# Kernel tuning notes

Measured on AMD Instinct MI355X. Metric: run time of the kernel, lower is better.

## Reference

```python
import jax, jax.numpy as jnp
import numpy as np

HEAD_SIZE = 64
EMB_SIZE = 1024
B, N = 4, 4096


def setup_inputs() -> dict:
    key = jax.random.key(0)
    kx, kk, kq, kv = jax.random.split(key, 4)
    x = jax.random.normal(kx, (B, N, EMB_SIZE), dtype=jnp.float32)
    # nn.Linear(emb, head, bias=False): weight [head, emb]; y = x @ W.T
    s = 1.0 / np.sqrt(EMB_SIZE)
    Wk = jax.random.uniform(kk, (HEAD_SIZE, EMB_SIZE), jnp.float32, -s, s)
    Wq = jax.random.uniform(kq, (HEAD_SIZE, EMB_SIZE), jnp.float32, -s, s)
    Wv = jax.random.uniform(kv, (HEAD_SIZE, EMB_SIZE), jnp.float32, -s, s)
    return {"x": x, "Wk": Wk, "Wq": Wq, "Wv": Wv}


def reference(x, Wk, Wq, Wv):
    # k, q, v: [B, N, H]
    k = jnp.einsum("bne,he->bnh", x, Wk)
    q = jnp.einsum("bne,he->bnh", x, Wq)
    v = jnp.einsum("bne,he->bnh", x, Wv)
    scale = HEAD_SIZE ** -0.5
    aff = jnp.einsum("bqh,bkh->bqk", q, k) * scale  # [B, N, N]
    aff = jax.nn.softmax(aff, axis=2)
    # dropout rate is 0.0 -> identity
    return jnp.einsum("bqk,bkh->bqh", aff, v)
```

## Files before the change

kernel.cpp:

```cpp
#include <hip/hip_runtime.h>

#define NB   4
#define SEQ  4096
#define EMB  1024
#define HS   64

typedef __attribute__((ext_vector_type(8))) short bf16x8;
typedef __attribute__((ext_vector_type(4))) float f32x4;

__device__ inline unsigned short f2bf(float f) {
  unsigned int u = __float_as_uint(f);
  u += 0x7fffu + ((u >> 16) & 1u);
  return (unsigned short)(u >> 16);
}
__device__ inline float bf2f(unsigned short h) {
  return __uint_as_float(((unsigned int)h) << 16);
}
__device__ inline int swzi64(int row, int c) {
  return row * 64 + ((c ^ (row & 7)) << 3);
}
__device__ inline int swzi32(int row, int c) {
  return row * 32 + ((c ^ ((row >> 1) & 3)) << 3);
}
__device__ inline int swzi128(int row, int c) {
  return row * 128 + ((c ^ (row & 7)) << 3);
}
__device__ inline void gld16(const unsigned short* g, unsigned short* l) {
  __builtin_amdgcn_global_load_lds(
      (const __attribute__((address_space(1))) void*)g,
      (__attribute__((address_space(3))) void*)l, 16, 0, 0);
}

__global__ __launch_bounds__(256) void wprep(
    const float* __restrict__ Wk, const float* __restrict__ Wq,
    const float* __restrict__ Wv,
    unsigned short* __restrict__ Wh, unsigned short* __restrict__ Wl) {
  int i = blockIdx.x * 256 + threadIdx.x;
  int e = i >> 8, c = i & 255;
  float4 v;
  float sc = 1.0f;
  if (e < 64)       { v = ((const float4*)Wq)[e * 256 + c];
                      sc = 0.18033688011112042f; }
  else if (e < 128)   v = ((const float4*)Wk)[(e - 64) * 256 + c];
  else                v = ((const float4*)Wv)[(e - 128) * 256 + c];
  v.x *= sc; v.y *= sc; v.z *= sc; v.w *= sc;
  ushort4 hv, lv;
  hv.x = f2bf(v.x); lv.x = f2bf(v.x - bf2f(hv.x));
  hv.y = f2bf(v.y); lv.y = f2bf(v.y - bf2f(hv.y));
  hv.z = f2bf(v.z); lv.z = f2bf(v.z - bf2f(hv.z));
  hv.w = f2bf(v.w); lv.w = f2bf(v.w - bf2f(hv.w));
  *(ushort4*)&Wh[i * 4] = hv;
  *(ushort4*)&Wl[i * 4] = lv;
}

#define XhSp(p) ((unsigned short*)(SM + (p) * 2048))
#define XlSp(p) ((unsigned short*)(SM + 4096 + (p) * 2048))
#define WhSp(p) ((unsigned short*)(SM + 8192 + (p) * 12288))
#define WlSp(p) ((unsigned short*)(SM + 32768 + (p) * 12288))

__global__ __launch_bounds__(256) void qkv_x1(
    const float* __restrict__ x,
    const unsigned short* __restrict__ Wh, const unsigned short* __restrict__ Wl,
    unsigned short* __restrict__ qh, unsigned short* __restrict__ ql,
    unsigned short* __restrict__ kh, unsigned short* __restrict__ kl,
    unsigned short* __restrict__ vt) {
  __shared__ __align__(16) unsigned char SM[57344];

  const int t  = threadIdx.x;
  const int l  = t & 63;
  const int li = l & 15;
  const int g  = l >> 4;
  const int w  = t >> 6;
  const int m0 = blockIdx.x * 32;
  const int b  = m0 >> 12;
  const int n0 = m0 & 4095;

  const int xrow = t >> 3;
  const float* xp = x + (m0 + xrow) * EMB + (t & 7) * 4;
  const int xaddr = xrow * 32 + ((((t & 7) >> 1) ^ ((xrow >> 1) & 3)) << 3)
                    + (t & 1) * 4;

  const int wconst = (l >> 2) * EMB + (((l & 3) ^ ((l >> 3) & 3)) << 3);

  f32x4 acc[2][3];
#pragma unroll
  for (int i = 0; i < 2; ++i)
#pragma unroll
    for (int j = 0; j < 3; ++j) acc[i][j] = (f32x4){0.f, 0.f, 0.f, 0.f};

  const int rA0 = li, rA1 = 16 + li;
  const int rB0 = 48 * w + li, rB1 = rB0 + 16, rB2 = rB0 + 32;

  auto issueW = [&](int s, int p) {
    const int ko = s * 32;
#pragma unroll
    for (int i = 0; i < 3; ++i) {
      const int seg = 3 * w + i;
      gld16(Wh + 16 * seg * EMB + wconst + ko, WhSp(p) + seg * 512);
      gld16(Wl + 16 * seg * EMB + wconst + ko, WlSp(p) + seg * 512);
    }
  };
  auto writeX = [&](float4 v, int p) {
    unsigned short h0 = f2bf(v.x), h1 = f2bf(v.y), h2 = f2bf(v.z), h3 = f2bf(v.w);
    unsigned short e0 = f2bf(v.x - bf2f(h0)), e1 = f2bf(v.y - bf2f(h1));
    unsigned short e2 = f2bf(v.z - bf2f(h2)), e3 = f2bf(v.w - bf2f(h3));
    int2 hv, lv;
    hv.x = (int)((unsigned)h0 | ((unsigned)h1 << 16));
    hv.y = (int)((unsigned)h2 | ((unsigned)h3 << 16));
    lv.x = (int)((unsigned)e0 | ((unsigned)e1 << 16));
    lv.y = (int)((unsigned)e2 | ((unsigned)e3 << 16));
    *(int2*)&XhSp(p)[xaddr] = hv;
    *(int2*)&XlSp(p)[xaddr] = lv;
  };

  float4 px = *(const float4*)xp;
  issueW(0, 0);
  writeX(px, 0);
  px = *(const float4*)(xp + 32);
  __syncthreads();

  for (int s = 0; s < 32; ++s) {
    const int p = s & 1;
    if (s < 31) {
      issueW(s + 1, p ^ 1);
      writeX(px, p ^ 1);
      if (s < 30) px = *(const float4*)(xp + (s + 2) * 32);
    } else {
      asm volatile("s_waitcnt vmcnt(0)" ::: "memory");
    }
    __builtin_amdgcn_sched_barrier(0);

    bf16x8 ah0 = *(const bf16x8*)&XhSp(p)[swzi32(rA0, g)];
    bf16x8 ah1 = *(const bf16x8*)&XhSp(p)[swzi32(rA1, g)];
    bf16x8 al0 = *(const bf16x8*)&XlSp(p)[swzi32(rA0, g)];
    bf16x8 al1 = *(const bf16x8*)&XlSp(p)[swzi32(rA1, g)];
    bf16x8 bh0 = *(const bf16x8*)&WhSp(p)[swzi32(rB0, g)];
    bf16x8 bh1 = *(const bf16x8*)&WhSp(p)[swzi32(rB1, g)];
    bf16x8 bh2 = *(const bf16x8*)&WhSp(p)[swzi32(rB2, g)];
    bf16x8 bl0 = *(const bf16x8*)&WlSp(p)[swzi32(rB0, g)];
    bf16x8 bl1 = *(const bf16x8*)&WlSp(p)[swzi32(rB1, g)];
    bf16x8 bl2 = *(const bf16x8*)&WlSp(p)[swzi32(rB2, g)];

    __builtin_amdgcn_s_setprio(1);
    acc[0][0] = __builtin_amdgcn_mfma_f32_16x16x32_bf16(ah0, bh0, acc[0][0], 0,0,0);
    acc[0][0] = __builtin_amdgcn_mfma_f32_16x16x32_bf16(ah0, bl0, acc[0][0], 0,0,0);
    acc[0][0] = __builtin_amdgcn_mfma_f32_16x16x32_bf16(al0, bh0, acc[0][0], 0,0,0);
    acc[0][1] = __builtin_amdgcn_mfma_f32_16x16x32_bf16(ah0, bh1, acc[0][1], 0,0,0);
    acc[0][1] = __builtin_amdgcn_mfma_f32_16x16x32_bf16(ah0, bl1, acc[0][1], 0,0,0);
    acc[0][1] = __builtin_amdgcn_mfma_f32_16x16x32_bf16(al0, bh1, acc[0][1], 0,0,0);
    acc[0][2] = __builtin_amdgcn_mfma_f32_16x16x32_bf16(ah0, bh2, acc[0][2], 0,0,0);
    acc[0][2] = __builtin_amdgcn_mfma_f32_16x16x32_bf16(ah0, bl2, acc[0][2], 0,0,0);
    acc[0][2] = __builtin_amdgcn_mfma_f32_16x16x32_bf16(al0, bh2, acc[0][2], 0,0,0);
    acc[1][0] = __builtin_amdgcn_mfma_f32_16x16x32_bf16(ah1, bh0, acc[1][0], 0,0,0);
    acc[1][0] = __builtin_amdgcn_mfma_f32_16x16x32_bf16(ah1, bl0, acc[1][0], 0,0,0);
    acc[1][0] = __builtin_amdgcn_mfma_f32_16x16x32_bf16(al1, bh0, acc[1][0], 0,0,0);
    acc[1][1] = __builtin_amdgcn_mfma_f32_16x16x32_bf16(ah1, bh1, acc[1][1], 0,0,0);
    acc[1][1] = __builtin_amdgcn_mfma_f32_16x16x32_bf16(ah1, bl1, acc[1][1], 0,0,0);
    acc[1][1] = __builtin_amdgcn_mfma_f32_16x16x32_bf16(al1, bh1, acc[1][1], 0,0,0);
    acc[1][2] = __builtin_amdgcn_mfma_f32_16x16x32_bf16(ah1, bh2, acc[1][2], 0,0,0);
    acc[1][2] = __builtin_amdgcn_mfma_f32_16x16x32_bf16(ah1, bl2, acc[1][2], 0,0,0);
    acc[1][2] = __builtin_amdgcn_mfma_f32_16x16x32_bf16(al1, bh2, acc[1][2], 0,0,0);
    __builtin_amdgcn_s_setprio(0);

    asm volatile("s_waitcnt lgkmcnt(0)" ::: "memory");
    __builtin_amdgcn_s_barrier();
    __builtin_amdgcn_sched_barrier(0);
  }

#pragma unroll
  for (int i = 0; i < 2; ++i)
#pragma unroll
    for (int j = 0; j < 3; ++j) {
      const int H3 = 48 * w + 16 * j + li;
#pragma unroll
      for (int r = 0; r < 4; ++r) {
        const int mrow = 16 * i + 4 * g + r;
        const float vv = acc[i][j][r];
        if (H3 < 64) {
          const unsigned short hb = f2bf(vv);
          const int off = (b * SEQ + n0 + mrow) * HS + H3;
          qh[off] = hb; ql[off] = f2bf(vv - bf2f(hb));
        } else if (H3 < 128) {
          const unsigned short hb = f2bf(vv);
          const int off = (b * SEQ + n0 + mrow) * HS + (H3 - 64);
          kh[off] = hb; kl[off] = f2bf(vv - bf2f(hb));
        } else {
          vt[(b * HS + (H3 - 128)) * SEQ + n0 + mrow] = f2bf(vv);
        }
      }
    }
}

__global__ __launch_bounds__(1024) void attn_mfma(
    const unsigned short* __restrict__ qh, const unsigned short* __restrict__ ql,
    const unsigned short* __restrict__ kh, const unsigned short* __restrict__ kl,
    const unsigned short* __restrict__ vt, float* __restrict__ out) {
  __shared__ __align__(16) unsigned char SM[155648];
  unsigned short* const PtS = (unsigned short*)(SM + 114688);

  const int t  = threadIdx.x;
  const int l  = t & 63;
  const int li = l & 15;
  const int g  = l >> 4;
  const int w  = t >> 6;
  const int qg = w & 1;
  const int kf = w >> 1;
  const int ks2 = (w >> 1) & 3;
  const int hh  = w >> 3;
  const int b  = blockIdx.y;
  const int q0 = blockIdx.x << 6;

  bf16x8 qfh[2][2], qfl[2][2];
#pragma unroll
  for (int qs = 0; qs < 2; ++qs) {
    const unsigned short* qrh = qh + (b * SEQ + q0 + 32 * qg + 16 * qs + li) * HS;
    const unsigned short* qrl = ql + (b * SEQ + q0 + 32 * qg + 16 * qs + li) * HS;
    qfh[qs][0] = *(const bf16x8*)&qrh[8 * g];
    qfh[qs][1] = *(const bf16x8*)&qrh[32 + 8 * g];
    qfl[qs][0] = *(const bf16x8*)&qrl[8 * g];
    qfl[qs][1] = *(const bf16x8*)&qrl[32 + 8 * g];
  }

  const int kconst = (l >> 3) * HS + (((l & 7) ^ (l >> 3)) << 3);
  const int rowl = l >> 4, slot = l & 15;
  const int vc = (w & 1) ? rowl * SEQ + ((slot ^ (4 + rowl)) << 3)
                         : rowl * SEQ + ((slot ^ rowl) << 3);
  const unsigned short* khB = kh + b * SEQ * HS;
  const unsigned short* klB = kl + b * SEQ * HS;
  const unsigned short* vtB = vt + b * HS * SEQ;

  f32x4 O[2][2];
#pragma unroll
  for (int i = 0; i < 2; ++i) {
    O[i][0] = (f32x4){0.f, 0.f, 0.f, 0.f};
    O[i][1] = (f32x4){0.f, 0.f, 0.f, 0.f};
  }
  float lp0 = 0.f, lp1 = 0.f;

  const int slabW = qg + 2 * (kf >> 1);
  const int cW = 2 * (kf & 1) + (g >> 1);
  const int subW = (g & 1) << 2;

  auto stage = [&](int it, int pK, int vb) {
    const int kt0 = it << 7;
    unsigned short* const KhP = (unsigned short*)(SM + pK * 16384);
    unsigned short* const KlP = (unsigned short*)(SM + 32768 + pK * 16384);
    unsigned short* const VtP = (unsigned short*)(SM + 65536 + vb * 16384);
    gld16(khB + (kt0 + 8 * w) * HS + kconst, KhP + w * 512);
    gld16(klB + (kt0 + 8 * w) * HS + kconst, KlP + w * 512);
    gld16(vtB + 4 * w * SEQ + kt0 + vc, VtP + w * 512);
  };

  auto PV = [&](int par, int vb) {
    unsigned short* const PtP = PtS + (qg + 2 * ks2) * 2560 + par * 1280;
    unsigned short* const VtP = (unsigned short*)(SM + 65536 + vb * 16384);
    bf16x8 pb0 = *(const bf16x8*)&PtP[li * 40 + ((g ^ (li & 3)) << 3)];
    const int r1 = 16 + li;
    bf16x8 pb1 = *(const bf16x8*)&PtP[r1 * 40 + ((g ^ (r1 & 3)) << 3)];
    __builtin_amdgcn_s_setprio(1);
#pragma unroll
    for (int ht2 = 0; ht2 < 2; ++ht2) {
      const int vrow = 32 * hh + 16 * ht2 + li;
      bf16x8 va = *(const bf16x8*)&VtP[swzi128(vrow, 4 * ks2 + g)];
      O[ht2][0] = __builtin_amdgcn_mfma_f32_16x16x32_bf16(va, pb0, O[ht2][0], 0,0,0);
      O[ht2][1] = __builtin_amdgcn_mfma_f32_16x16x32_bf16(va, pb1, O[ht2][1], 0,0,0);
    }
    __builtin_amdgcn_s_setprio(0);
  };

  stage(0, 0, 0);
  __syncthreads();

  int vbn = 1;
  int vbp = 2;
  for (int it = 0; it < 32; ++it) {
    const int p = it & 1;
    if (it < 31) stage(it + 1, p ^ 1, vbn);

    unsigned short* const KhS = (unsigned short*)(SM + p * 16384);
    unsigned short* const KlS = (unsigned short*)(SM + 32768 + p * 16384);

    f32x4 S[2];
    S[0] = (f32x4){-32.f, -32.f, -32.f, -32.f};
    S[1] = (f32x4){-32.f, -32.f, -32.f, -32.f};
    __builtin_amdgcn_s_setprio(1);
#pragma unroll
    for (int khf = 0; khf < 2; ++khf) {
      const int row = 16 * kf + li;
      bf16x8 akh = *(const bf16x8*)&KhS[swzi64(row, 4 * khf + g)];
      bf16x8 akl = *(const bf16x8*)&KlS[swzi64(row, 4 * khf + g)];
      S[0] = __builtin_amdgcn_mfma_f32_16x16x32_bf16(akh, qfh[0][khf], S[0], 0,0,0);
      S[0] = __builtin_amdgcn_mfma_f32_16x16x32_bf16(akh, qfl[0][khf], S[0], 0,0,0);
      S[0] = __builtin_amdgcn_mfma_f32_16x16x32_bf16(akl, qfh[0][khf], S[0], 0,0,0);
      S[1] = __builtin_amdgcn_mfma_f32_16x16x32_bf16(akh, qfh[1][khf], S[1], 0,0,0);
      S[1] = __builtin_amdgcn_mfma_f32_16x16x32_bf16(akh, qfl[1][khf], S[1], 0,0,0);
      S[1] = __builtin_amdgcn_mfma_f32_16x16x32_bf16(akl, qfh[1][khf], S[1], 0,0,0);
    }
    __builtin_amdgcn_s_setprio(0);

    if (it > 0) PV(p ^ 1, vbp);

#pragma unroll
    for (int qs = 0; qs < 2; ++qs) {
      unsigned pu[4];
      float ls = 0.f;
#pragma unroll
      for (int r = 0; r < 4; ++r) {
        const float pe = exp2f(S[qs][r]);
        pu[r] = __float_as_uint(pe);
        ls += __uint_as_float(pu[r] & 0xffff0000u);
      }
      if (qs == 0) lp0 += ls; else lp1 += ls;
      const unsigned p01 = __builtin_amdgcn_perm(pu[1], pu[0], 0x07060302u);
      const unsigned p23 = __builtin_amdgcn_perm(pu[3], pu[2], 0x07060302u);
      const int qrow = 16 * qs + li;
      const int addr = qrow * 40 + (((cW ^ (qrow & 3))) << 3) + subW;
      int2 pv; pv.x = (int)p01; pv.y = (int)p23;
      *(int2*)&PtS[slabW * 2560 + p * 1280 + addr] = pv;
    }

    __syncthreads();

    vbn = (vbn == 2) ? 0 : vbn + 1;
    vbp = (vbp == 2) ? 0 : vbp + 1;
  }

  PV(1, 1);

  lp0 += __shfl_xor(lp0, 16); lp0 += __shfl_xor(lp0, 32);
  lp1 += __shfl_xor(lp1, 16); lp1 += __shfl_xor(lp1, 32);

  float* const OTm = (float*)SM;
  float* const Lm  = (float*)(SM + 65536);
#pragma unroll
  for (int ht2 = 0; ht2 < 2; ++ht2)
#pragma unroll
    for (int qs = 0; qs < 2; ++qs) {
      float4 o4;
      o4.x = O[ht2][qs][0]; o4.y = O[ht2][qs][1];
      o4.z = O[ht2][qs][2]; o4.w = O[ht2][qs][3];
      *(float4*)&OTm[(((qg * 2 + hh) * 4 + ks2) << 10)
                     + (16 * qs + li) * 32 + 16 * ht2 + 4 * g] = o4;
    }
  if (g == 0) { Lm[w * 32 + li] = lp0; Lm[w * 32 + 16 + li] = lp1; }
  __syncthreads();

  {
    const int q = t >> 4, hseg = (t & 15) << 2;
    const int qq = q & 31, qgf = q >> 5;
    const int hhf = hseg >> 5, hsub = hseg & 31;
    float lF = 0.f;
#pragma unroll
    for (int kff = 0; kff < 8; ++kff) lF += Lm[(qgf + 2 * kff) * 32 + qq];
    float4 a = {0.f, 0.f, 0.f, 0.f};
#pragma unroll
    for (int k2 = 0; k2 < 4; ++k2) {
      const float* Ob = OTm + (((qgf * 2 + hhf) * 4 + k2) << 10) + qq * 32 + hsub;
      float4 u = *(const float4*)Ob;
      a.x += u.x; a.y += u.y; a.z += u.z; a.w += u.w;
    }
    const float inv = 1.f / lF;
    a.x *= inv; a.y *= inv; a.z *= inv; a.w *= inv;
    *(float4*)(out + (b * SEQ + q0 + q) * HS + hseg) = a;
  }
}

extern "C" void kernel_launch(void* const* d_in, const int* in_sizes, int n_in,
                              void* d_out, int out_size, void* d_ws,
                              size_t ws_size, hipStream_t stream) {
  const float* x  = (const float*)d_in[0];
  const float* Wk = (const float*)d_in[1];
  const float* Wq = (const float*)d_in[2];
  const float* Wv = (const float*)d_in[3];
  float* out = (float*)d_out;

  unsigned short* us = (unsigned short*)d_ws;
  unsigned short* qh = us + 0 * (1 << 20);
  unsigned short* ql = us + 1 * (1 << 20);
  unsigned short* kh = us + 2 * (1 << 20);
  unsigned short* kl = us + 3 * (1 << 20);
  unsigned short* vt = us + 4 * (1 << 20);
  unsigned short* Wh = us + 5 * (1 << 20);
  unsigned short* Wl = Wh + 192 * 1024;

  wprep<<<192, 256, 0, stream>>>(Wk, Wq, Wv, Wh, Wl);
  qkv_x1<<<512, 256, 0, stream>>>(x, Wh, Wl, qh, ql, kh, kl, vt);
  attn_mfma<<<dim3(64, NB), 1024, 0, stream>>>(qh, ql, kh, kl, vt, out);
}
```

Before: 177.6 us.

## Halve QKV projection row tile and load low-part weights directly into registers

The QKV projection kernel now processes 16 rows per block instead of 32 and launches 1024 blocks. The low-precision weight half now goes straight from global memory into registers, double-buffered across steps, instead of being staged in LDS. Together these halve shared memory per block and add a launch-bounds occupancy hint, aiming for more resident blocks and better latency hiding. In exchange, each block's weight loads are reused over fewer rows, so global and L2 traffic for the weights doubles.

```diff
diff --git a/kernel.cpp b/kernel.cpp
--- a/kernel.cpp
+++ b/kernel.cpp
@@ -53,42 +53,43 @@
   *(ushort4*)&Wl[i * 4] = lv;
 }
 
-#define XhSp(p) ((unsigned short*)(SM + (p) * 2048))
-#define XlSp(p) ((unsigned short*)(SM + 4096 + (p) * 2048))
-#define WhSp(p) ((unsigned short*)(SM + 8192 + (p) * 12288))
-#define WlSp(p) ((unsigned short*)(SM + 32768 + (p) * 12288))
-
-__global__ __launch_bounds__(256) void qkv_x1(
+#define XhSp(p) ((unsigned short*)(SM + (p) * 1024))
+#define XlSp(p) ((unsigned short*)(SM + 2048 + (p) * 1024))
+#define WhSp(p) ((unsigned short*)(SM + 4096 + (p) * 12288))
+
+__global__ __launch_bounds__(256, 4) void qkv_x1(
     const float* __restrict__ x,
     const unsigned short* __restrict__ Wh, const unsigned short* __restrict__ Wl,
     unsigned short* __restrict__ qh, unsigned short* __restrict__ ql,
     unsigned short* __restrict__ kh, unsigned short* __restrict__ kl,
     unsigned short* __restrict__ vt) {
-  __shared__ __align__(16) unsigned char SM[57344];
+  __shared__ __align__(16) unsigned char SM[28672];
 
   const int t  = threadIdx.x;
   const int l  = t & 63;
   const int li = l & 15;
   const int g  = l >> 4;
   const int w  = t >> 6;
-  const int m0 = blockIdx.x * 32;
+  const int m0 = blockIdx.x * 16;
   const int b  = m0 >> 12;
   const int n0 = m0 & 4095;
 
-  const int xrow = t >> 3;
-  const float* xp = x + (m0 + xrow) * EMB + (t & 7) * 4;
-  const int xaddr = xrow * 32 + ((((t & 7) >> 1) ^ ((xrow >> 1) & 3)) << 3)
-                    + (t & 1) * 4;
+  const int xrow = t >> 4;
+  const int c2   = t & 15;
+  const float* xp = x + (m0 + xrow) * EMB + 2 * c2;
+  const int xaddr = xrow * 32 + (((c2 >> 2) ^ ((xrow >> 1) & 3)) << 3)
+                    + (c2 & 3) * 2;
 
   const int wconst = (l >> 2) * EMB + (((l & 3) ^ ((l >> 3) & 3)) << 3);
 
-  f32x4 acc[2][3];
-#pragma unroll
-  for (int i = 0; i < 2; ++i)
-#pragma unroll
-    for (int j = 0; j < 3; ++j) acc[i][j] = (f32x4){0.f, 0.f, 0.f, 0.f};
-
-  const int rA0 = li, rA1 = 16 + li;
+  const unsigned short* const WlR0 = Wl + (48 * w + li) * EMB + 8 * g;
+  const unsigned short* const WlR1 = Wl + (48 * w + 16 + li) * EMB + 8 * g;
+  const unsigned short* const WlR2 = Wl + (48 * w + 32 + li) * EMB + 8 * g;
+
+  f32x4 acc[3];
+#pragma unroll
+  for (int j = 0; j < 3; ++j) acc[j] = (f32x4){0.f, 0.f, 0.f, 0.f};
+
   const int rB0 = 48 * w + li, rB1 = rB0 + 16, rB2 = rB0 + 32;
 
   auto issueW = [&](int s, int p) {
@@ -97,98 +98,88 @@
     for (int i = 0; i < 3; ++i) {
       const int seg = 3 * w + i;
       gld16(Wh + 16 * seg * EMB + wconst + ko, WhSp(p) + seg * 512);
-      gld16(Wl + 16 * seg * EMB + wconst + ko, WlSp(p) + seg * 512);
-    }
-  };
-  auto writeX = [&](float4 v, int p) {
-    unsigned short h0 = f2bf(v.x), h1 = f2bf(v.y), h2 = f2bf(v.z), h3 = f2bf(v.w);
+    }
+  };
+  auto loadBl = [&](int s, bf16x8 (&B)[3]) {
+    const int ko = s * 32;
+    B[0] = *(const bf16x8*)&WlR0[ko];
+    B[1] = *(const bf16x8*)&WlR1[ko];
+    B[2] = *(const bf16x8*)&WlR2[ko];
+  };
+  auto writeX = [&](float2 v, int p) {
+    unsigned short h0 = f2bf(v.x), h1 = f2bf(v.y);
     unsigned short e0 = f2bf(v.x - bf2f(h0)), e1 = f2bf(v.y - bf2f(h1));
-    unsigned short e2 = f2bf(v.z - bf2f(h2)), e3 = f2bf(v.w - bf2f(h3));
-    int2 hv, lv;
-    hv.x = (int)((unsigned)h0 | ((unsigned)h1 << 16));
-    hv.y = (int)((unsigned)h2 | ((unsigned)h3 << 16));
-    lv.x = (int)((unsigned)e0 | ((unsigned)e1 << 16));
-    lv.y = (int)((unsigned)e2 | ((unsigned)e3 << 16));
-    *(int2*)&XhSp(p)[xaddr] = hv;
-    *(int2*)&XlSp(p)[xaddr] = lv;
-  };
-
-  float4 px = *(const float4*)xp;
+    *(unsigned*)&XhSp(p)[xaddr] = (unsigned)h0 | ((unsigned)h1 << 16);
+    *(unsigned*)&XlSp(p)[xaddr] = (unsigned)e0 | ((unsigned)e1 << 16);
+  };
+
+  bf16x8 BlA[3], BlB[3];
   issueW(0, 0);
-  writeX(px, 0);
-  px = *(const float4*)(xp + 32);
+  loadBl(0, BlA);
+  writeX(*(const float2*)xp, 0);
+  float2 px = *(const float2*)(xp + 32);
   __syncthreads();
 
-  for (int s = 0; s < 32; ++s) {
+  auto step = [&](int s, bf16x8 (&Blc)[3], bf16x8 (&Bln)[3]) {
     const int p = s & 1;
     if (s < 31) {
       issueW(s + 1, p ^ 1);
+      loadBl(s + 1, Bln);
       writeX(px, p ^ 1);
-      if (s < 30) px = *(const float4*)(xp + (s + 2) * 32);
+      if (s < 30) px = *(const float2*)(xp + (s + 2) * 32);
     } else {
       asm volatile("s_waitcnt vmcnt(0)" ::: "memory");
     }
     __builtin_amdgcn_sched_barrier(0);
 
-    bf16x8 ah0 = *(const bf16x8*)&XhSp(p)[swzi32(rA0, g)];
-    bf16x8 ah1 = *(const bf16x8*)&XhSp(p)[swzi32(rA1, g)];
-    bf16x8 al0 = *(const bf16x8*)&XlSp(p)[swzi32(rA0, g)];
-    bf16x8 al1 = *(const bf16x8*)&XlSp(p)[swzi32(rA1, g)];
+    bf16x8 ah = *(const bf16x8*)&XhSp(p)[swzi32(li, g)];
+    bf16x8 al = *(const bf16x8*)&XlSp(p)[swzi32(li, g)];
     bf16x8 bh0 = *(const bf16x8*)&WhSp(p)[swzi32(rB0, g)];
     bf16x8 bh1 = *(const bf16x8*)&WhSp(p)[swzi32(rB1, g)];
     bf16x8 bh2 = *(const bf16x8*)&WhSp(p)[swzi32(rB2, g)];
-    bf16x8 bl0 = *(const bf16x8*)&WlSp(p)[swzi32(rB0, g)];
-    bf16x8 bl1 = *(const bf16x8*)&WlSp(p)[swzi32(rB1, g)];
-    bf16x8 bl2 = *(const bf16x8*)&WlSp(p)[swzi32(rB2, g)];
 
     __builtin_amdgcn_s_setprio(1);
-    acc[0][0] = __builtin_amdgcn_mfma_f32_16x16x32_bf16(ah0, bh0, acc[0][0], 0,0,0);
-    acc[0][0] = __builtin_amdgcn_mfma_f32_16x16x32_bf16(ah0, bl0, acc[0][0], 0,0,0);
-    acc[0][0] = __builtin_amdgcn_mfma_f32_16x16x32_bf16(al0, bh0, acc[0][0], 0,0,0);
-    acc[0][1] = __builtin_amdgcn_mfma_f32_16x16x32_bf16(ah0, bh1, acc[0][1], 0,0,0);
-    acc[0][1] = __builtin_amdgcn_mfma_f32_16x16x32_bf16(ah0, bl1, acc[0][1], 0,0,0);
-    acc[0][1] = __builtin_amdgcn_mfma_f32_16x16x32_bf16(al0, bh1, acc[0][1], 0,0,0);
-    acc[0][2] = __builtin_amdgcn_mfma_f32_16x16x32_bf16(ah0, bh2, acc[0][2], 0,0,0);
-    acc[0][2] = __builtin_amdgcn_mfma_f32_16x16x32_bf16(ah0, bl2, acc[0][2], 0,0,0);
-    acc[0][2] = __builtin_amdgcn_mfma_f32_16x16x32_bf16(al0, bh2, acc[0][2], 0,0,0);
-    acc[1][0] = __builtin_amdgcn_mfma_f32_16x16x32_bf16(ah1, bh0, acc[1][0], 0,0,0);
-    acc[1][0] = __builtin_amdgcn_mfma_f32_16x16x32_bf16(ah1, bl0, acc[1][0], 0,0,0);
-    acc[1][0] = __builtin_amdgcn_mfma_f32_16x16x32_bf16(al1, bh0, acc[1][0], 0,0,0);
-    acc[1][1] = __builtin_amdgcn_mfma_f32_16x16x32_bf16(ah1, bh1, acc[1][1], 0,0,0);
-    acc[1][1] = __builtin_amdgcn_mfma_f32_16x16x32_bf16(ah1, bl1, acc[1][1], 0,0,0);
-    acc[1][1] = __builtin_amdgcn_mfma_f32_16x16x32_bf16(al1, bh1, acc[1][1], 0,0,0);
-    acc[1][2] = __builtin_amdgcn_mfma_f32_16x16x32_bf16(ah1, bh2, acc[1][2], 0,0,0);
-    acc[1][2] = __builtin_amdgcn_mfma_f32_16x16x32_bf16(ah1, bl2, acc[1][2], 0,0,0);
-    acc[1][2] = __builtin_amdgcn_mfma_f32_16x16x32_bf16(al1, bh2, acc[1][2], 0,0,0);
+    acc[0] = __builtin_amdgcn_mfma_f32_16x16x32_bf16(ah, bh0,    acc[0], 0,0,0);
+    acc[0] = __builtin_amdgcn_mfma_f32_16x16x32_bf16(ah, Blc[0], acc[0], 0,0,0);
+    acc[0] = __builtin_amdgcn_mfma_f32_16x16x32_bf16(al, bh0,    acc[0], 0,0,0);
+    acc[1] = __builtin_amdgcn_mfma_f32_16x16x32_bf16(ah, bh1,    acc[1], 0,0,0);
+    acc[1] = __builtin_amdgcn_mfma_f32_16x16x32_bf16(ah, Blc[1], acc[1], 0,0,0);
+    acc[1] = __builtin_amdgcn_mfma_f32_16x16x32_bf16(al, bh1,    acc[1], 0,0,0);
+    acc[2] = __builtin_amdgcn_mfma_f32_16x16x32_bf16(ah, bh2,    acc[2], 0,0,0);
+    acc[2] = __builtin_amdgcn_mfma_f32_16x16x32_bf16(ah, Blc[2], acc[2], 0,0,0);
+    acc[2] = __builtin_amdgcn_mfma_f32_16x16x32_bf16(al, bh2,    acc[2], 0,0,0);
     __builtin_amdgcn_s_setprio(0);
 
     asm volatile("s_waitcnt lgkmcnt(0)" ::: "memory");
     __builtin_amdgcn_s_barrier();
     __builtin_amdgcn_sched_barrier(0);
-  }
-
-#pragma unroll
-  for (int i = 0; i < 2; ++i)
-#pragma unroll
-    for (int j = 0; j < 3; ++j) {
-      const int H3 = 48 * w + 16 * j + li;
-#pragma unroll
-      for (int r = 0; r < 4; ++r) {
-        const int mrow = 16 * i + 4 * g + r;
-        const float vv = acc[i][j][r];
-        if (H3 < 64) {
-          const unsigned short hb = f2bf(vv);
-          const int off = (b * SEQ + n0 + mrow) * HS + H3;
-          qh[off] = hb; ql[off] = f2bf(vv - bf2f(hb));
-        } else if (H3 < 128) {
-          const unsigned short hb = f2bf(vv);
-          const int off = (b * SEQ + n0 + mrow) * HS + (H3 - 64);
-          kh[off] = hb; kl[off] = f2bf(vv - bf2f(hb));
-        } else {
-          vt[(b * HS + (H3 - 128)) * SEQ + n0 + mrow] = f2bf(vv);
-        }
+  };
+
+  for (int s2 = 0; s2 < 16; ++s2) {
+    step(2 * s2,     BlA, BlB);
+    step(2 * s2 + 1, BlB, BlA);
+  }
+
+#pragma unroll
+  for (int j = 0; j < 3; ++j) {
+    const int H3 = 48 * w + 16 * j + li;
+#pragma unroll
+    for (int r = 0; r < 4; ++r) {
+      const int mrow = 4 * g + r;
+      const float vv = acc[j][r];
+      if (H3 < 64) {
+        const unsigned short hb = f2bf(vv);
+        const int off = (b * SEQ + n0 + mrow) * HS + H3;
+        qh[off] = hb; ql[off] = f2bf(vv - bf2f(hb));
+      } else if (H3 < 128) {
+        const unsigned short hb = f2bf(vv);
+        const int off = (b * SEQ + n0 + mrow) * HS + (H3 - 64);
+        kh[off] = hb; kl[off] = f2bf(vv - bf2f(hb));
+      } else {
+        vt[(b * HS + (H3 - 128)) * SEQ + n0 + mrow] = f2bf(vv);
       }
     }
+  }
 }
 
 __global__ __launch_bounds__(1024) void attn_mfma(
@@ -384,6 +375,6 @@
   unsigned short* Wl = Wh + 192 * 1024;
 
   wprep<<<192, 256, 0, stream>>>(Wk, Wq, Wv, Wh, Wl);
-  qkv_x1<<<512, 256, 0, stream>>>(x, Wh, Wl, qh, ql, kh, kl, vt);
+  qkv_x1<<<1024, 256, 0, stream>>>(x, Wh, Wl, qh, ql, kh, kl, vt);
   attn_mfma<<<dim3(64, NB), 1024, 0, stream>>>(qh, ql, kh, kl, vt, out);
 }
```

New measurement: 211.3 us. 1.19x slower.
